# Performance work log

Hardware: AMD Instinct MI355X
Metric: run time of the kernel (lower is better)

## Reference

```python
import jax, jax.numpy as jnp
import numpy as np

N_NODES = 50000
N_EDGES = 800000
H = 128
NUM_LAYERS = 4
NUM_CLASSES = 10
NUM_GRAPHS = 256


def setup_inputs() -> dict:
    key = jax.random.key(0)
    ks = jax.random.split(key, 12)
    s = 0.05
    x = jax.random.normal(ks[0], (N_NODES, H), dtype=jnp.float32)
    edge_index = jax.random.randint(ks[1], (2, N_EDGES), 0, N_NODES, dtype=jnp.int32)
    batch = jnp.sort(jax.random.randint(ks[2], (N_NODES,), 0, NUM_GRAPHS, dtype=jnp.int32))
    W = jax.random.normal(ks[3], (NUM_LAYERS, H, H), dtype=jnp.float32) * s
    gru_w_ih = jax.random.normal(ks[4], (3 * H, H), dtype=jnp.float32) * s
    gru_w_hh = jax.random.normal(ks[5], (3 * H, H), dtype=jnp.float32) * s
    gru_b_ih = jax.random.normal(ks[6], (3 * H,), dtype=jnp.float32) * s
    gru_b_hh = jax.random.normal(ks[7], (3 * H,), dtype=jnp.float32) * s
    local_w = jax.random.normal(ks[8], (H, H), dtype=jnp.float32) * s
    local_b = jax.random.normal(ks[9], (H,), dtype=jnp.float32) * s
    global_w = jax.random.normal(ks[10], (NUM_CLASSES, H), dtype=jnp.float32) * s
    global_b = jax.random.normal(ks[11], (NUM_CLASSES,), dtype=jnp.float32) * s
    return {"x": x, "edge_index": edge_index, "batch": batch, "W": W,
            "gru_w_ih": gru_w_ih, "gru_w_hh": gru_w_hh,
            "gru_b_ih": gru_b_ih, "gru_b_hh": gru_b_hh,
            "local_w": local_w, "local_b": local_b,
            "global_w": global_w, "global_b": global_b}


def _gru_cell(a, h, w_ih, w_hh, b_ih, b_hh):
    # torch.nn.GRUCell math; gate order r, z, n
    gi = a @ w_ih.T + b_ih
    gh = h @ w_hh.T + b_hh
    i_r, i_z, i_n = jnp.split(gi, 3, axis=-1)
    h_r, h_z, h_n = jnp.split(gh, 3, axis=-1)
    r = jax.nn.sigmoid(i_r + h_r)
    z = jax.nn.sigmoid(i_z + h_z)
    n = jnp.tanh(i_n + r * h_n)
    return (1.0 - z) * n + z * h


def reference(x, edge_index, batch, W, gru_w_ih, gru_w_hh, gru_b_ih, gru_b_hh,
              local_w, local_b, global_w, global_b):
    n_nodes = x.shape[0]
    hidden = W.shape[-1]
    # GatedGraphConv pads input features up to hidden_dim
    h = x if x.shape[1] == hidden else jnp.pad(x, ((0, 0), (0, hidden - x.shape[1])))
    src, dst = edge_index[0], edge_index[1]  # messages flow src -> dst
    for l in range(W.shape[0]):
        m = h @ W[l]                                            # [N, H]
        aggr = jax.ops.segment_sum(m[src], dst, num_segments=n_nodes)  # gather+scatter-add
        h = _gru_cell(aggr, h, gru_w_ih, gru_w_hh, gru_b_ih, gru_b_hh)
    local = jax.nn.relu(h @ local_w.T + local_b)                # [N, H]
    sums = jax.ops.segment_sum(local, batch, num_segments=NUM_GRAPHS)   # [G, H]
    counts = jax.ops.segment_sum(jnp.ones((n_nodes, 1), local.dtype), batch,
                                 num_segments=NUM_GRAPHS)
    pooled = sums / jnp.maximum(counts, 1.0)                    # global_mean_pool
    out = pooled @ global_w.T + global_b                        # [G, C]
    return jax.nn.log_softmax(out, axis=-1)
```

## Files before the change

kernel.cpp:

```cpp
#include <hip/hip_runtime.h>

#define NN 50000
#define NE 800000
#define HD 128
#define NL 4
#define NC 10
#define NG 256
#define CAP 64

typedef __attribute__((ext_vector_type(8))) short short8;
typedef __attribute__((ext_vector_type(4))) float floatx4;

union frg { uint4 u; short8 s; };

__device__ __forceinline__ short8 load_frag(const ushort* p){
  frg f; f.u = *(const uint4*)p; return f.s;
}
__device__ __forceinline__ floatx4 MFMA(short8 a, short8 b, floatx4 c){
  return __builtin_amdgcn_mfma_f32_16x16x32_bf16(a, b, c, 0, 0, 0);
}

__device__ __forceinline__ ushort f2bf(float x){
  unsigned u = __float_as_uint(x);
  return (ushort)((u + 0x7FFFu + ((u >> 16) & 1u)) >> 16);
}
__device__ __forceinline__ float bf2f(ushort b){
  return __uint_as_float(((uint)b) << 16);
}
__device__ __forceinline__ float sigmf(float x){ return 1.0f/(1.0f + __expf(-x)); }
__device__ __forceinline__ float tanhff(float x){ return 2.0f/(1.0f + __expf(-2.0f*x)) - 1.0f; }

__global__ __launch_bounds__(256) void prep_weights_bf16(
    const float* __restrict__ w_hh, const float* __restrict__ local_w,
    const float* __restrict__ b_ih, const float* __restrict__ b_hh,
    ushort* __restrict__ whh_bf, ushort* __restrict__ lw_bf,
    float* __restrict__ bs)
{
  int idx = blockIdx.x*256 + threadIdx.x;
  if (idx < 49152) whh_bf[idx] = f2bf(w_hh[idx]);
  else if (idx < 65536){ int j = idx - 49152; lw_bf[j] = f2bf(local_w[j]); }
  else if (idx < 66048){
    int j = idx - 65536;
    if (j < 256)      bs[j] = b_ih[j] + b_hh[j];
    else if (j < 384) bs[j] = b_ih[j];
    else              bs[j] = b_hh[j - 128];
  }
}

__global__ __launch_bounds__(256) void veff_kernel(
    const float* __restrict__ W, const float* __restrict__ w_ih,
    ushort* __restrict__ veffT)
{
  int idx = blockIdx.x*256 + threadIdx.x;
  if (idx >= 4*49152) return;
  int l = idx / 49152, rem = idx % 49152;
  int o = rem >> 7, j = rem & 127;
  const float4* wr = (const float4*)&W[(size_t)(l*128 + j)*128];
  const float4* ir = (const float4*)&w_ih[(size_t)o*128];
  float acc = 0.f;
  #pragma unroll
  for (int q = 0; q < 32; q++){
    float4 a = wr[q], b = ir[q];
    acc += a.x*b.x + a.y*b.y + a.z*b.z + a.w*b.w;
  }
  veffT[idx] = f2bf(acc);
}

__global__ __launch_bounds__(256) void convert_x(const float4* __restrict__ x, ushort4* __restrict__ xbf)
{
  int i = blockIdx.x*256 + threadIdx.x;
  if (i < NN*HD/4){
    float4 v = x[i];
    ushort4 o; o.x=f2bf(v.x); o.y=f2bf(v.y); o.z=f2bf(v.z); o.w=f2bf(v.w);
    xbf[i] = o;
  }
}

__global__ __launch_bounds__(256) void fill_csr_direct(
    const int* __restrict__ src, const int* __restrict__ dst,
    int* deg, int* __restrict__ csrf)
{
  int e = blockIdx.x*256 + threadIdx.x;
  if (e < NE){
    int s = __builtin_nontemporal_load(&src[e]);
    int d = __builtin_nontemporal_load(&dst[e]);
    int pos = atomicAdd(&deg[d], 1);
    if (pos < CAP) csrf[(d << 6) + pos] = s;
  }
}

__global__ __launch_bounds__(64) void graph_ptr_kernel(const int* __restrict__ batch, int* __restrict__ gptr)
{
  int g = blockIdx.x*64 + threadIdx.x;
  if (g > NG) return;
  int lo = 0, hi = NN;
  while (lo < hi){
    int mid = (lo + hi) >> 1;
    if (batch[mid] < g) lo = mid + 1; else hi = mid;
  }
  gptr[g] = lo;
}

__global__ __launch_bounds__(256) void aggregate_bf16(
    const uint4* __restrict__ m4, const int* __restrict__ deg,
    const int* __restrict__ csrf, uint4* __restrict__ aggr4)
{
  int t = threadIdx.x;
  int lane16 = t & 15;
  int nid = blockIdx.x*16 + (t >> 4);
  int cnt = deg[nid]; if (cnt > CAP) cnt = CAP;
  const int* lst = csrf + (nid << 6);
  float a0=0.f,a1=0.f,a2=0.f,a3=0.f,a4=0.f,a5=0.f,a6=0.f,a7=0.f;
  int j = 0;
  for (; j + 3 < cnt; j += 4){
    int i0 = lst[j], i1 = lst[j+1], i2 = lst[j+2], i3 = lst[j+3];
    uint4 v0 = m4[(size_t)i0*16 + lane16];
    uint4 v1 = m4[(size_t)i1*16 + lane16];
    uint4 v2 = m4[(size_t)i2*16 + lane16];
    uint4 v3 = m4[(size_t)i3*16 + lane16];
    a0 += __uint_as_float(v0.x << 16) + __uint_as_float(v1.x << 16)
        + __uint_as_float(v2.x << 16) + __uint_as_float(v3.x << 16);
    a1 += __uint_as_float(v0.x & 0xFFFF0000u) + __uint_as_float(v1.x & 0xFFFF0000u)
        + __uint_as_float(v2.x & 0xFFFF0000u) + __uint_as_float(v3.x & 0xFFFF0000u);
    a2 += __uint_as_float(v0.y << 16) + __uint_as_float(v1.y << 16)
        + __uint_as_float(v2.y << 16) + __uint_as_float(v3.y << 16);
    a3 += __uint_as_float(v0.y & 0xFFFF0000u) + __uint_as_float(v1.y & 0xFFFF0000u)
        + __uint_as_float(v2.y & 0xFFFF0000u) + __uint_as_float(v3.y & 0xFFFF0000u);
    a4 += __uint_as_float(v0.z << 16) + __uint_as_float(v1.z << 16)
        + __uint_as_float(v2.z << 16) + __uint_as_float(v3.z << 16);
    a5 += __uint_as_float(v0.z & 0xFFFF0000u) + __uint_as_float(v1.z & 0xFFFF0000u)
        + __uint_as_float(v2.z & 0xFFFF0000u) + __uint_as_float(v3.z & 0xFFFF0000u);
    a6 += __uint_as_float(v0.w << 16) + __uint_as_float(v1.w << 16)
        + __uint_as_float(v2.w << 16) + __uint_as_float(v3.w << 16);
    a7 += __uint_as_float(v0.w & 0xFFFF0000u) + __uint_as_float(v1.w & 0xFFFF0000u)
        + __uint_as_float(v2.w & 0xFFFF0000u) + __uint_as_float(v3.w & 0xFFFF0000u);
  }
  for (; j < cnt; j++){
    int s = lst[j];
    uint4 v = m4[(size_t)s*16 + lane16];
    a0 += __uint_as_float(v.x << 16);
    a1 += __uint_as_float(v.x & 0xFFFF0000u);
    a2 += __uint_as_float(v.y << 16);
    a3 += __uint_as_float(v.y & 0xFFFF0000u);
    a4 += __uint_as_float(v.z << 16);
    a5 += __uint_as_float(v.z & 0xFFFF0000u);
    a6 += __uint_as_float(v.w << 16);
    a7 += __uint_as_float(v.w & 0xFFFF0000u);
  }
  uint4 o;
  o.x = (uint)f2bf(a0) | ((uint)f2bf(a1) << 16);
  o.y = (uint)f2bf(a2) | ((uint)f2bf(a3) << 16);
  o.z = (uint)f2bf(a4) | ((uint)f2bf(a5) << 16);
  o.w = (uint)f2bf(a6) | ((uint)f2bf(a7) << 16);
  aggr4[(size_t)nid*16 + lane16] = o;
}

__global__ __launch_bounds__(256, 2) void gru_mfma4(
    const ushort* __restrict__ sumh_bf, ushort* __restrict__ h_bf_out,
    const ushort* __restrict__ h_bf_in,
    const ushort* __restrict__ veffT, const ushort* __restrict__ whh_bf,
    const float* __restrict__ bs)
{
  __shared__ __align__(16) ushort lds_in[16384];
  __shared__ __align__(16) ushort lds_out[64*136];
  int t = threadIdx.x;
  int wv = t >> 6, lane = t & 63;
  int mrow = lane & 15, quad = lane >> 4;
  int nb = blockIdx.x * 64;

  #pragma unroll
  for (int q = 0; q < 8; q++){
    int c = wv*8 + q;
    int arr = c >> 4, tt = (c >> 2) & 3, kc = c & 3;
    const ushort* srcb = arr ? h_bf_in : sumh_bf;
    int node = nb + tt*16 + mrow; if (node >= NN) node = NN-1;
    uint4 v = *(const uint4*)&srcb[(size_t)node*HD + kc*32 + quad*8];
    *(uint4*)&lds_in[c*512 + lane*8] = v;
  }
  __syncthreads();

  floatx4 aR[4][2] = {}, aZ[4][2] = {}, aIN[4][2] = {}, aHN[4][2] = {};

  #pragma unroll
  for (int kc = 0; kc < 4; kc++){
    int k0 = kc*32 + quad*8;
    short8 fa[4], fh[4];
    #pragma unroll
    for (int tt = 0; tt < 4; tt++){
      fa[tt] = load_frag(&lds_in[((tt<<2) | kc)*512 + lane*8]);
      fh[tt] = load_frag(&lds_in[(16 | (tt<<2) | kc)*512 + lane*8]);
    }
    #pragma unroll
    for (int ftl = 0; ftl < 2; ftl++){
      size_t wo = (size_t)((wv*2 + ftl)*16 + mrow)*HD + k0;
      short8 vir = load_frag(&veffT[wo]);
      short8 viz = load_frag(&veffT[128*HD + wo]);
      short8 vin = load_frag(&veffT[256*HD + wo]);
      short8 whr = load_frag(&whh_bf[wo]);
      short8 whz = load_frag(&whh_bf[128*HD + wo]);
      short8 whn = load_frag(&whh_bf[256*HD + wo]);
      #pragma unroll
      for (int tt = 0; tt < 4; tt++){
        aR[tt][ftl]  = MFMA(fa[tt], vir, aR[tt][ftl]);
        aR[tt][ftl]  = MFMA(fh[tt], whr, aR[tt][ftl]);
        aZ[tt][ftl]  = MFMA(fa[tt], viz, aZ[tt][ftl]);
        aZ[tt][ftl]  = MFMA(fh[tt], whz, aZ[tt][ftl]);
        aIN[tt][ftl] = MFMA(fa[tt], vin, aIN[tt][ftl]);
        aHN[tt][ftl] = MFMA(fh[tt], whn, aHN[tt][ftl]);
      }
    }
  }

  #pragma unroll
  for (int ftl = 0; ftl < 2; ftl++){
    int feat = wv*32 + ftl*16 + mrow;
    float br  = bs[feat], bz = bs[128+feat], bin = bs[256+feat], bhn = bs[384+feat];
    int kw = ftl*16 + mrow;
    int qq = kw >> 3, jj = kw & 7;
    #pragma unroll
    for (int tt = 0; tt < 4; tt++){
      int cho = (16 | (tt<<2) | wv)*512;
      #pragma unroll
      for (int r = 0; r < 4; r++){
        int nrow = quad*4 + r;
        float rr = sigmf(aR[tt][ftl][r] + br);
        float zz = sigmf(aZ[tt][ftl][r] + bz);
        float nn = tanhff(aIN[tt][ftl][r] + bin + rr*(aHN[tt][ftl][r] + bhn));
        float ho = bf2f(lds_in[cho + (qq*16 + nrow)*8 + jj]);
        float hv = (1.f - zz)*nn + zz*ho;
        lds_out[(tt*16 + nrow)*136 + feat] = f2bf(hv);
      }
    }
  }
  __syncthreads();

  #pragma unroll
  for (int p = 0; p < 4; p++){
    int chunk = p*256 + t;
    int node = chunk >> 4, f = (chunk & 15)*8;
    int ng = nb + node;
    if (ng < NN){
      uint4 v = *(const uint4*)&lds_out[node*136 + f];
      *(uint4*)&h_bf_out[(size_t)ng*HD + f] = v;
    }
  }
}

__global__ __launch_bounds__(256) void local_gemm_mfma(
    const ushort* __restrict__ hbf, const ushort* __restrict__ lw_bf,
    const float* __restrict__ bias, float* __restrict__ local)
{
  int wv = threadIdx.x >> 6, lane = threadIdx.x & 63;
  int mt = blockIdx.x*4 + wv;
  if (mt >= NN/16) return;
  int m0 = mt*16, mrow = lane & 15, quad = lane >> 4;
  floatx4 acc[8] = {};
  for (int kc = 0; kc < 4; kc++){
    int k0 = kc*32 + quad*8;
    short8 a = load_frag(&hbf[(size_t)(m0 + mrow)*HD + k0]);
    #pragma unroll
    for (int ft = 0; ft < 8; ft++){
      short8 b = load_frag(&lw_bf[(size_t)(ft*16 + mrow)*HD + k0]);
      acc[ft] = MFMA(a, b, acc[ft]);
    }
  }
  #pragma unroll
  for (int ft = 0; ft < 8; ft++){
    float bv = bias[ft*16 + mrow];
    #pragma unroll
    for (int r = 0; r < 4; r++){
      int n = m0 + quad*4 + r;
      local[(size_t)n*HD + ft*16 + mrow] = fmaxf(acc[ft][r] + bv, 0.f);
    }
  }
}

__global__ __launch_bounds__(256) void pool_kernel(
    const float* __restrict__ local, const int* __restrict__ gptr,
    float* __restrict__ pooled)
{
  __shared__ float4 red[8][32];
  int g = blockIdx.x;
  int lane = threadIdx.x & 31;
  int st = threadIdx.x >> 5;
  int s0 = gptr[g], s1 = gptr[g+1];
  float4 acc = make_float4(0,0,0,0);
  for (int n = s0 + st; n < s1; n += 8){
    float4 v = *(const float4*)&local[(size_t)n*HD + lane*4];
    acc.x += v.x; acc.y += v.y; acc.z += v.z; acc.w += v.w;
  }
  red[st][lane] = acc;
  __syncthreads();
  if (st == 0){
    float4 s = red[0][lane];
    #pragma unroll
    for (int i=1;i<8;i++){
      float4 v = red[i][lane];
      s.x += v.x; s.y += v.y; s.z += v.z; s.w += v.w;
    }
    float cnt = (float)(s1 - s0);
    if (cnt < 1.0f) cnt = 1.0f;
    float inv = 1.0f / cnt;
    s.x *= inv; s.y *= inv; s.z *= inv; s.w *= inv;
    *(float4*)&pooled[g*HD + lane*4] = s;
  }
}

__global__ __launch_bounds__(64) void classifier_kernel(
    const float* __restrict__ pooled,
    const float* __restrict__ gw, const float* __restrict__ gb,
    float* __restrict__ out)
{
  int g = blockIdx.x;
  int lane = threadIdx.x;
  float p0 = pooled[g*HD + lane];
  float p1 = pooled[g*HD + 64 + lane];
  float vals[NC];
  #pragma unroll
  for (int c=0;c<NC;c++){
    float s = p0*gw[c*HD + lane] + p1*gw[c*HD + 64 + lane];
    #pragma unroll
    for (int off=32; off>0; off>>=1) s += __shfl_down(s, off, 64);
    vals[c] = s;
  }
  if (lane == 0){
    float mx = -1e30f;
    #pragma unroll
    for (int c=0;c<NC;c++){ vals[c] += gb[c]; mx = fmaxf(mx, vals[c]); }
    float se = 0.f;
    #pragma unroll
    for (int c=0;c<NC;c++) se += __expf(vals[c] - mx);
    float lse = mx + __logf(se);
    #pragma unroll
    for (int c=0;c<NC;c++) out[g*NC + c] = vals[c] - lse;
  }
}

extern "C" void kernel_launch(void* const* d_in, const int* in_sizes, int n_in,
                              void* d_out, int out_size, void* d_ws, size_t ws_size,
                              hipStream_t stream)
{
  const float* x        = (const float*)d_in[0];
  const int*   ei       = (const int*)  d_in[1];
  const int*   batch    = (const int*)  d_in[2];
  const float* W        = (const float*)d_in[3];
  const float* w_ih     = (const float*)d_in[4];
  const float* w_hh     = (const float*)d_in[5];
  const float* b_ih     = (const float*)d_in[6];
  const float* b_hh     = (const float*)d_in[7];
  const float* local_w  = (const float*)d_in[8];
  const float* local_b  = (const float*)d_in[9];
  const float* global_w = (const float*)d_in[10];
  const float* global_b = (const float*)d_in[11];
  float* out = (float*)d_out;

  char* base = (char*)d_ws;
  int*    csr_fixed = (int*)base;
  char*   R       = base + 25600000;
  ushort* sumh_bf = (ushort*)R;
  ushort* veffT   = (ushort*)(R + 12800000);
  ushort* whh_bf  = (ushort*)(R + 13193216);
  float*  bsums   = (float*)(R + 13291520);
  float*  local   = (float*)R;
  ushort* xbf     = (ushort*)(base + 51200000);
  ushort* hbf     = (ushort*)(base + 64000000);
  ushort* lw_bf   = (ushort*)(base + 76800000);
  float*  pooled  = (float*)(base + 76832768);
  int* deg        = (int*)(base + 76963840);
  int* gptr       = deg + NN;

  const int* esrc = ei;
  const int* edst = ei + NE;

  hipMemsetAsync(deg, 0, NN*sizeof(int), stream);
  prep_weights_bf16<<<259, 256, 0, stream>>>(w_hh, local_w, b_ih, b_hh, whh_bf, lw_bf, bsums);
  veff_kernel<<<768, 256, 0, stream>>>(W, w_ih, veffT);
  convert_x<<<6250, 256, 0, stream>>>((const float4*)x, (ushort4*)xbf);
  fill_csr_direct<<<3125, 256, 0, stream>>>(esrc, edst, deg, csr_fixed);
  graph_ptr_kernel<<<5, 64, 0, stream>>>(batch, gptr);

  const ushort* hin_b = xbf;
  for (int l = 0; l < NL; l++){
    aggregate_bf16<<<3125, 256, 0, stream>>>((const uint4*)hin_b, deg, csr_fixed, (uint4*)sumh_bf);
    gru_mfma4<<<782, 256, 0, stream>>>(sumh_bf, hbf, hin_b,
                                       veffT + (size_t)l*49152, whh_bf, bsums);
    hin_b = hbf;
  }

  local_gemm_mfma<<<782, 256, 0, stream>>>(hbf, lw_bf, local_b, local);
  pool_kernel<<<NG, 256, 0, stream>>>(local, gptr, pooled);
  classifier_kernel<<<NG, 64, 0, stream>>>(pooled, global_w, global_b, out);
}
```

Before: 478.1 us.

## Slice CSR build by destination range per XCD and store 16-bit indices

The CSR fill kernel now splits destination nodes into 8 ranges, one per blockIdx mod 8. Every edge chunk is scanned by 8 blocks, and each keeps only edges whose destination falls in its range. The intent is to keep atomics and scattered CSR writes local to one L2/XCD slice. Neighbor indices are also stored as 16-bit values, since node ids fit below 65536, which halves CSR footprint and the index reads in aggregation. The cost is reading the dst array 8 times and dropping nontemporal loads.

Measured after the change: 472.4 us. Within noise of the previous version (-1.2%).

```diff
diff --git a/kernel.cpp b/kernel.cpp
--- a/kernel.cpp
+++ b/kernel.cpp
@@ -76,16 +76,25 @@
   }
 }
 
-__global__ __launch_bounds__(256) void fill_csr_direct(
+#define NSLICE 8
+#define CHUNKS 400
+#define EPC (NE/CHUNKS)
+__global__ __launch_bounds__(256) void fill_csr_sliced(
     const int* __restrict__ src, const int* __restrict__ dst,
-    int* deg, int* __restrict__ csrf)
-{
-  int e = blockIdx.x*256 + threadIdx.x;
-  if (e < NE){
-    int s = __builtin_nontemporal_load(&src[e]);
-    int d = __builtin_nontemporal_load(&dst[e]);
-    int pos = atomicAdd(&deg[d], 1);
-    if (pos < CAP) csrf[(d << 6) + pos] = s;
+    int* deg, ushort* __restrict__ csrf)
+{
+  int slice = blockIdx.x & (NSLICE-1);
+  int chunk = blockIdx.x >> 3;
+  int e0 = chunk * EPC;
+  int lo = slice * (NN/NSLICE);
+  int hi = lo + (NN/NSLICE);
+  for (int e = e0 + threadIdx.x; e < e0 + EPC; e += 256){
+    int d = dst[e];
+    if (d >= lo && d < hi){
+      int s = src[e];
+      int pos = atomicAdd(&deg[d], 1);
+      if (pos < CAP) csrf[(d << 6) + pos] = (ushort)s;
+    }
   }
 }
 
@@ -103,13 +112,13 @@
 
 __global__ __launch_bounds__(256) void aggregate_bf16(
     const uint4* __restrict__ m4, const int* __restrict__ deg,
-    const int* __restrict__ csrf, uint4* __restrict__ aggr4)
+    const ushort* __restrict__ csrf, uint4* __restrict__ aggr4)
 {
   int t = threadIdx.x;
   int lane16 = t & 15;
   int nid = blockIdx.x*16 + (t >> 4);
   int cnt = deg[nid]; if (cnt > CAP) cnt = CAP;
-  const int* lst = csrf + (nid << 6);
+  const ushort* lst = csrf + (nid << 6);
   float a0=0.f,a1=0.f,a2=0.f,a3=0.f,a4=0.f,a5=0.f,a6=0.f,a7=0.f;
   int j = 0;
   for (; j + 3 < cnt; j += 4){
@@ -355,7 +364,7 @@
   float* out = (float*)d_out;
 
   char* base = (char*)d_ws;
-  int*    csr_fixed = (int*)base;
+  ushort* csr_fixed = (ushort*)base;
   char*   R       = base + 25600000;
   ushort* sumh_bf = (ushort*)R;
   ushort* veffT   = (ushort*)(R + 12800000);
@@ -376,7 +385,7 @@
   prep_weights_bf16<<<259, 256, 0, stream>>>(w_hh, local_w, b_ih, b_hh, whh_bf, lw_bf, bsums);
   veff_kernel<<<768, 256, 0, stream>>>(W, w_ih, veffT);
   convert_x<<<6250, 256, 0, stream>>>((const float4*)x, (ushort4*)xbf);
-  fill_csr_direct<<<3125, 256, 0, stream>>>(esrc, edst, deg, csr_fixed);
+  fill_csr_sliced<<<NSLICE*CHUNKS, 256, 0, stream>>>(esrc, edst, deg, csr_fixed);
   graph_ptr_kernel<<<5, 64, 0, stream>>>(batch, gptr);
 
   const ushort* hin_b = xbf;
```
